# Kernel optimization log

Hardware: AMD Instinct MI355X
Metric: run time of the kernel (lower is better)

The kernel has to match this reference:

```python
import jax, jax.numpy as jnp
import numpy as np


def _gat(x, adj, W, a):
    # x: [N, J, Fin], W: [H, Fin, hs], a: [H, 2*hs]
    # e_ij = leakyrelu(a1.Wh_i + a2.Wh_j)  (decomposed form of the repeat/cat construction)
    hs = W.shape[-1]
    Wh = jnp.einsum('bjf,hfd->bhjd', x, W)
    s1 = jnp.einsum('bhjd,hd->bhj', Wh, a[:, :hs])
    s2 = jnp.einsum('bhjd,hd->bhj', Wh, a[:, hs:])
    e = jax.nn.leaky_relu(s1[..., :, None] + s2[..., None, :], 0.2)
    e = jnp.where(adj[None, None] > 0, e, jnp.float32(-9e15))
    att = jax.nn.softmax(e, axis=-1)
    h = jnp.einsum('bhij,bhjd->bhid', att, Wh)
    b, H, j, d = h.shape
    return jax.nn.elu(h.transpose(0, 2, 1, 3).reshape(b, j, H * d))


def _conv_bn_relu(x, w, bias, g, be, m, v):
    # x: [N, C, T], w: [O, I, 3], BN in inference mode
    y = jax.lax.conv_general_dilated(x, w, (1,), [(1, 1)], dimension_numbers=('NCH', 'OIH', 'NCH'))
    y = y + bias[None, :, None]
    y = (y - m[None, :, None]) / jnp.sqrt(v[None, :, None] + 1e-5) * g[None, :, None] + be[None, :, None]
    return jax.nn.relu(y)


def _mha(q, k, v, wq, bq, wk, bk, wv, bv, wo, bo):
    # torch nn.MultiheadAttention, 4 heads, eval mode (no dropout)
    n, L, D = q.shape
    H = 4
    hd = D // H
    def proj(x, w, b):
        return (x @ w.T + b).reshape(n, -1, H, hd)
    Q, K, V = proj(q, wq, bq), proj(k, wk, bk), proj(v, wv, bv)
    att = jax.nn.softmax(jnp.einsum('nqhd,nkhd->nhqk', Q, K) * jnp.float32(1.0 / np.sqrt(hd)), axis=-1)
    o = jnp.einsum('nhqk,nkhd->nqhd', att, V).reshape(n, L, D)
    return o @ wo.T + bo


def _lstm_dir(x, wih, whh, bih, bhh, rev):
    # x: [B, T, D]; torch gate order i, f, g, o
    b, t, _ = x.shape
    H = whh.shape[1]
    xw = jnp.transpose(x @ wih.T + (bih + bhh), (1, 0, 2))  # [T, B, 4H]
    def step(carry, xt):
        h, c = carry
        gates = xt + h @ whh.T
        i, f, g, o = jnp.split(gates, 4, axis=-1)
        c = jax.nn.sigmoid(f) * c + jax.nn.sigmoid(i) * jnp.tanh(g)
        h = jax.nn.sigmoid(o) * jnp.tanh(c)
        return (h, c), h
    init = (jnp.zeros((b, H), x.dtype), jnp.zeros((b, H), x.dtype))
    _, hs = jax.lax.scan(step, init, xw, reverse=rev)
    return jnp.transpose(hs, (1, 0, 2))


def _forward(lh, rh, adj, vis, g1W, g1a, g2W, g2a, c1w, c1b, b1g, b1b, b1m, b1v, c2w, c2b, b2g, b2b, b2m, b2v,
             wq, bq, wk, bk, wv, bv, wo, bo,
             l0fw, l0fu, l0fbi, l0fbh, l0bw, l0bu, l0bbi, l0bbh,
             l1fw, l1fu, l1fbi, l1fbh, l1bw, l1bu, l1bbi, l1bbh,
             o1w, o1b, o2w, o2b):
    B, T, J, F = lh.shape

    def single_hand(x):
        h = x.reshape(B * T, J, F)
        h = _gat(h, adj, g1W, g1a)
        h = _gat(h, adj, g2W, g2a)
        D = h.shape[-1]
        ht = h.reshape(B, T, J, D).transpose(0, 2, 3, 1).reshape(B * J, D, T)
        ht = _conv_bn_relu(ht, c1w, c1b, b1g, b1b, b1m, b1v)
        ht = _conv_bn_relu(ht, c2w, c2b, b2g, b2b, b2m, b2v)
        return ht.reshape(B, J, D, T).transpose(0, 3, 1, 2)  # [B, T, J, D]

    l = single_hand(lh)
    r = single_hand(rh)
    D = l.shape[-1]
    lf = l.reshape(B * T, J, D)
    rf = r.reshape(B * T, J, D)
    a_l2r = _mha(lf, rf, rf, wq, bq, wk, bk, wv, bv, wo, bo)
    a_r2l = _mha(rf, lf, lf, wq, bq, wk, bk, wv, bv, wo, bo)
    # repair of shape-inconsistent torch reshape: pool joints before the seq LSTM
    le = (lf + 0.5 * a_r2l).reshape(B, T, J, D).mean(axis=2)
    re = (rf + 0.5 * a_l2r).reshape(B, T, J, D).mean(axis=2)

    def bilstm(x):
        h1 = jnp.concatenate([_lstm_dir(x, l0fw, l0fu, l0fbi, l0fbh, False),
                              _lstm_dir(x, l0bw, l0bu, l0bbi, l0bbh, True)], -1)
        return jnp.concatenate([_lstm_dir(h1, l1fw, l1fu, l1fbi, l1fbh, False),
                                _lstm_dir(h1, l1bw, l1bu, l1bbi, l1bbh, True)], -1)

    def head(x):
        y = jax.nn.relu(x @ o1w.T + o1b) @ o2w.T + o2b  # [B, T, 3*J]
        return y.reshape(B, T, J, 3)

    lp = head(bilstm(le)) * vis[..., None]
    rp = head(bilstm(re)) * vis[..., None]
    return lp, rp


def setup_inputs() -> dict:
    key = jax.random.key(0)
    ks = jax.random.split(key, 60)
    it = iter(range(60))
    B, T, J, F, D = 8, 512, 21, 512, 256
    def nrm(shape, s=0.05):
        return jax.random.normal(ks[next(it)], shape, jnp.float32) * s
    inp = {}
    inp['left_hand_feats'] = nrm((B, T, J, F), 1.0)
    inp['right_hand_feats'] = nrm((B, T, J, F), 1.0)
    adj = (jax.random.uniform(ks[next(it)], (J, J)) < 0.3).astype(jnp.float32)
    inp['hand_adj_matrix'] = jnp.maximum(adj, jnp.eye(J, dtype=jnp.float32))
    inp['hand_visibility'] = jax.random.uniform(ks[next(it)], (B, T, J), jnp.float32)
    inp['gat1_W'] = nrm((4, F, 64)); inp['gat1_a'] = nrm((4, 128))
    inp['gat2_W'] = nrm((4, D, 64)); inp['gat2_a'] = nrm((4, 128))
    inp['conv1_w'] = nrm((D, D, 3)); inp['conv1_b'] = nrm((D,))
    inp['conv2_w'] = nrm((D, D, 3)); inp['conv2_b'] = nrm((D,))
    for p in ['bn1', 'bn2']:
        inp[p + '_g'] = jnp.ones((D,), jnp.float32)
        inp[p + '_b'] = jnp.zeros((D,), jnp.float32)
        inp[p + '_m'] = jnp.zeros((D,), jnp.float32)
        inp[p + '_v'] = jnp.ones((D,), jnp.float32)
    for p in ['attn_wq', 'attn_wk', 'attn_wv', 'attn_wo']:
        inp[p] = nrm((D, D))
    for p in ['attn_bq', 'attn_bk', 'attn_bv', 'attn_bo']:
        inp[p] = nrm((D,))
    H = D // 2
    for l in ['lstm0f', 'lstm0b', 'lstm1f', 'lstm1b']:
        inp[l + '_wih'] = nrm((4 * H, D))
        inp[l + '_whh'] = nrm((4 * H, H))
        inp[l + '_bih'] = nrm((4 * H,))
        inp[l + '_bhh'] = nrm((4 * H,))
    inp['out1_w'] = nrm((D, D)); inp['out1_b'] = nrm((D,))
    inp['out2_w'] = nrm((3 * J, D)); inp['out2_b'] = nrm((3 * J,))
    return inp


def reference(left_hand_feats, right_hand_feats, hand_adj_matrix, hand_visibility,
              gat1_W, gat1_a, gat2_W, gat2_a,
              conv1_w, conv1_b, bn1_g, bn1_b, bn1_m, bn1_v,
              conv2_w, conv2_b, bn2_g, bn2_b, bn2_m, bn2_v,
              attn_wq, attn_bq, attn_wk, attn_bk, attn_wv, attn_bv, attn_wo, attn_bo,
              lstm0f_wih, lstm0f_whh, lstm0f_bih, lstm0f_bhh,
              lstm0b_wih, lstm0b_whh, lstm0b_bih, lstm0b_bhh,
              lstm1f_wih, lstm1f_whh, lstm1f_bih, lstm1f_bhh,
              lstm1b_wih, lstm1b_whh, lstm1b_bih, lstm1b_bhh,
              out1_w, out1_b, out2_w, out2_b):
    return _forward(left_hand_feats, right_hand_feats, hand_adj_matrix, hand_visibility,
                    gat1_W, gat1_a, gat2_W, gat2_a,
                    conv1_w, conv1_b, bn1_g, bn1_b, bn1_m, bn1_v,
                    conv2_w, conv2_b, bn2_g, bn2_b, bn2_m, bn2_v,
                    attn_wq, attn_bq, attn_wk, attn_bk, attn_wv, attn_bv, attn_wo, attn_bo,
                    lstm0f_wih, lstm0f_whh, lstm0f_bih, lstm0f_bhh,
                    lstm0b_wih, lstm0b_whh, lstm0b_bih, lstm0b_bhh,
                    lstm1f_wih, lstm1f_whh, lstm1f_bih, lstm1f_bhh,
                    lstm1b_wih, lstm1b_whh, lstm1b_bih, lstm1b_bhh,
                    out1_w, out1_b, out2_w, out2_b)
```

## Files before the change

kernel.cpp:

```cpp
#include <hip/hip_runtime.h>

typedef __bf16 bf16;
typedef bf16 bf16x8 __attribute__((ext_vector_type(8)));
typedef bf16 bf16x4 __attribute__((ext_vector_type(4)));
typedef float f32x4 __attribute__((ext_vector_type(4)));
typedef _Float16 f16;
typedef f16 f16x8 __attribute__((ext_vector_type(8)));

#define NBT 4096
#define NJ 21
#define NLF 86016
#define DD 256
#define CONV_M 86352
#define SPAD 514
#define CROWS 86528

__device__ __forceinline__ void gload16(const bf16* g, bf16* l) {
  __builtin_amdgcn_global_load_lds(
      (const __attribute__((address_space(1))) unsigned int*)g,
      (__attribute__((address_space(3))) unsigned int*)l, 16, 0, 0);
}

__global__ __launch_bounds__(256, 2) void gemm_bf16(
    const void* __restrict__ Av, const bf16* __restrict__ Bt,
    float* __restrict__ C32, bf16* __restrict__ Cout,
    const float* __restrict__ bias, const float* __restrict__ sc,
    const float* __restrict__ sh, int M, int N, int K, int lda, int flags)
{
  __shared__ __align__(16) bf16 As[128][32];
  __shared__ __align__(16) bf16 Bs[128][32];
  const int tid = threadIdx.x;
  const long m0 = (long)blockIdx.y * 128;
  const int n0 = blockIdx.x * 128;
  const int wave = tid >> 6, lane = tid & 63;
  const int wm = (wave & 1) * 64, wn = (wave >> 1) * 64;
  const int frow = lane & 15, fkb = (lane >> 4) * 8;
  const int crow = lane >> 2, ccol = (lane & 3) * 8;
  f32x4 acc[4][4] = {};
  for (int k0 = 0; k0 < K; k0 += 32) {
    if (flags & 1) {
      const int lr = tid >> 1, lc = (tid & 1) * 16;
      const float* ap = (const float*)Av + (m0 + lr) * (long)lda + (k0 + lc);
      bf16x8 t0, t1;
      #pragma unroll
      for (int u = 0; u < 8; u++) { t0[u] = (bf16)ap[u]; t1[u] = (bf16)ap[8 + u]; }
      *(bf16x8*)(&As[lr][lc])     = t0;
      *(bf16x8*)(&As[lr][lc + 8]) = t1;
    } else {
      #pragma unroll
      for (int cc = 0; cc < 2; cc++) {
        const int ch = wave * 2 + cc;
        gload16((const bf16*)Av + (m0 + ch * 16 + crow) * (long)lda + (k0 + ccol),
                &As[ch * 16][0]);
      }
    }
    #pragma unroll
    for (int cc = 0; cc < 2; cc++) {
      const int ch = wave * 2 + cc;
      gload16(Bt + (n0 + ch * 16 + crow) * (long)K + (k0 + ccol),
              &Bs[ch * 16][0]);
    }
    __syncthreads();
    bf16x8 af[4], bg[4];
    #pragma unroll
    for (int i = 0; i < 4; i++) af[i] = *(const bf16x8*)(&As[wm + i * 16 + frow][fkb]);
    #pragma unroll
    for (int j = 0; j < 4; j++) bg[j] = *(const bf16x8*)(&Bs[wn + j * 16 + frow][fkb]);
    #pragma unroll
    for (int i = 0; i < 4; i++)
      #pragma unroll
      for (int j = 0; j < 4; j++)
        acc[i][j] = __builtin_amdgcn_mfma_f32_16x16x32_bf16(af[i], bg[j], acc[i][j], 0, 0, 0);
    __syncthreads();
  }
  const int col = lane & 15, rbase = (lane >> 4) * 4;
  #pragma unroll
  for (int i = 0; i < 4; i++) {
    #pragma unroll
    for (int j = 0; j < 4; j++) {
      const int nn = n0 + wn + j * 16 + col;
      #pragma unroll
      for (int r = 0; r < 4; r++) {
        const long mm = m0 + wm + i * 16 + rbase + r;
        if (mm >= M) continue;
        float v = acc[i][j][r];
        if (flags & 2) { C32[mm * (long)N + nn] = v; continue; }
        if (flags & 8) v = v * sc[nn] + sh[nn];
        else if (bias) v += bias[nn];
        if (flags & 4) v = fmaxf(v, 0.f);
        if (flags & 16) {
          const int s = (int)(mm % SPAD);
          if (s == 0 || s == SPAD - 1) v = 0.f;
          Cout[mm * (long)N + nn] = (bf16)v;
        } else if (flags & 32) {
          const long hj = mm / SPAD; const int s = (int)(mm - hj * SPAD);
          if (s == 0 || s == SPAD - 1) continue;
          const long b = hj / NJ; const int j2 = (int)(hj - b * NJ);
          const long dst = (b * 512 + (s - 1)) * NJ + j2;
          Cout[dst * (long)N + nn] = (bf16)v;
        } else {
          Cout[mm * (long)N + nn] = (bf16)v;
        }
      }
    }
  }
}

__global__ void cvt_k(const float* __restrict__ s, bf16* __restrict__ d, long n) {
  long i = (long)blockIdx.x * 256 + threadIdx.x;
  if (i < n) d[i] = (bf16)s[i];
}
__global__ void cvt4_k(const float* __restrict__ s, bf16* __restrict__ d, long n4) {
  long i = (long)blockIdx.x * 256 + threadIdx.x;
  if (i >= n4) return;
  const f32x4 v = ((const f32x4*)s)[i];
  bf16x4 o; o[0] = (bf16)v[0]; o[1] = (bf16)v[1]; o[2] = (bf16)v[2]; o[3] = (bf16)v[3];
  ((bf16x4*)d)[i] = o;
}
__global__ void prep_gatW(const float* __restrict__ W, bf16* __restrict__ Wt, int F) {
  long idx = (long)blockIdx.x * 256 + threadIdx.x;
  if (idx >= 256L * F) return;
  int n = (int)(idx / F), f = (int)(idx % F);
  Wt[idx] = (bf16)W[((long)(n >> 6) * F + f) * 64 + (n & 63)];
}
__global__ void prep_convw(const float* __restrict__ w, bf16* __restrict__ wp) {
  int idx = blockIdx.x * 256 + threadIdx.x;
  int n = idx / 768, k = idx % 768, tap = k >> 8, i = k & 255;
  wp[idx] = (bf16)w[(n * 256 + i) * 3 + tap];
}
__global__ void prep_out2(const float* __restrict__ w, bf16* __restrict__ wp) {
  int idx = blockIdx.x * 256 + threadIdx.x;
  wp[idx] = (idx < 63 * 256) ? (bf16)w[idx] : (bf16)0.f;
}
__global__ void prep_scsh(const float* __restrict__ cb, const float* __restrict__ g,
                          const float* __restrict__ be, const float* __restrict__ m,
                          const float* __restrict__ v, float* __restrict__ sc,
                          float* __restrict__ sh) {
  int c = threadIdx.x;
  float rs = rsqrtf(v[c] + 1e-5f) * g[c];
  sc[c] = rs; sh[c] = (cb[c] - m[c]) * rs + be[c];
}
__global__ void prep_bkv(const float* __restrict__ bk, const float* __restrict__ bv,
                         float* __restrict__ o) {
  int i = blockIdx.x * 256 + threadIdx.x;
  if (i >= 512) return;
  o[i] = (i < 256) ? bk[i] : bv[i - 256];
}
__global__ void pad_zero(bf16* __restrict__ convIn) {
  int idx = blockIdx.x * 256 + threadIdx.x;
  int hj = idx >> 9, s = ((idx >> 8) & 1) ? (SPAD - 1) : 0, c = idx & 255;
  convIn[((long)hj * SPAD + s) * DD + c] = (bf16)0.f;
}
__global__ void zero_out(float* __restrict__ o, long n) {
  long i = (long)blockIdx.x * 256 + threadIdx.x;
  if (i < n) o[i] = 0.f;
}

__global__ __launch_bounds__(256) void gat_attn(
    const bf16* __restrict__ Wh, const float* __restrict__ a,
    const float* __restrict__ adj, bf16* __restrict__ out, int convMode)
{
  const int bt = blockIdx.x, tid = threadIdx.x;
  __shared__ float whs[NJ][DD];
  __shared__ float s1[4][NJ], s2[4][NJ];
  __shared__ float att[4][NJ][NJ];
  const long base = (long)bt * NJ * DD;
  for (int i = tid; i < NJ * DD; i += 256)
    whs[i >> 8][i & 255] = (float)Wh[base + i];
  __syncthreads();
  if (tid < 4 * NJ) {
    const int h = tid / NJ, i = tid % NJ;
    float x1 = 0.f, x2 = 0.f;
    for (int d = 0; d < 64; d++) {
      const float w = whs[i][h * 64 + d];
      x1 += w * a[h * 128 + d];
      x2 += w * a[h * 128 + 64 + d];
    }
    s1[h][i] = x1; s2[h][i] = x2;
  }
  __syncthreads();
  for (int idx = tid; idx < 4 * NJ * NJ; idx += 256) {
    const int h = idx / (NJ * NJ), r = idx % (NJ * NJ), i = r / NJ, j = r % NJ;
    float e = s1[h][i] + s2[h][j];
    e = e > 0.f ? e : 0.2f * e;
    att[h][i][j] = (adj[i * NJ + j] > 0.f) ? e : -9e15f;
  }
  __syncthreads();
  if (tid < 4 * NJ) {
    const int h = tid / NJ, i = tid % NJ;
    float mx = -3e38f;
    for (int j = 0; j < NJ; j++) mx = fmaxf(mx, att[h][i][j]);
    float sum = 0.f;
    for (int j = 0; j < NJ; j++) { const float ex = __expf(att[h][i][j] - mx); att[h][i][j] = ex; sum += ex; }
    const float inv = 1.f / sum;
    for (int j = 0; j < NJ; j++) att[h][i][j] *= inv;
  }
  __syncthreads();
  const int b = bt >> 9, t = bt & 511;
  for (int idx = tid; idx < NJ * DD; idx += 256) {
    const int i = idx >> 8, c = idx & 255, h = c >> 6;
    float s = 0.f;
    for (int j = 0; j < NJ; j++) s += att[h][i][j] * whs[j][c];
    s = s > 0.f ? s : (__expf(s) - 1.f);
    const long row = convMode ? (((long)(b * NJ + i)) * SPAD + (t + 1)) : ((long)bt * NJ + i);
    out[row * DD + c] = (bf16)s;
  }
}

__global__ __launch_bounds__(256) void mha_core2(
    const bf16* __restrict__ Q, const bf16* __restrict__ KV,
    bf16* __restrict__ O)
{
  const int bt = blockIdx.x, tid = threadIdx.x;
  __shared__ bf16 qs[NJ][DD], ks[NJ][DD], vs[NJ][DD];
  __shared__ float att[4][NJ][NJ];
  const long baseq = (long)bt * NJ * DD;
  const long basekv = (long)bt * NJ * 512;
  for (int i = tid; i < NJ * DD; i += 256) {
    const int r = i >> 8, c = i & 255;
    qs[r][c] = Q[baseq + i];
    ks[r][c] = KV[basekv + r * 512 + c];
    vs[r][c] = KV[basekv + r * 512 + 256 + c];
  }
  __syncthreads();
  for (int idx = tid; idx < 4 * NJ * NJ; idx += 256) {
    const int h = idx / (NJ * NJ), r = idx % (NJ * NJ), i = r / NJ, j = r % NJ;
    float s = 0.f;
    for (int d = 0; d < 64; d++) s += (float)qs[i][h * 64 + d] * (float)ks[j][h * 64 + d];
    att[h][i][j] = s * 0.125f;
  }
  __syncthreads();
  if (tid < 4 * NJ) {
    const int h = tid / NJ, i = tid % NJ;
    float mx = -3e38f;
    for (int j = 0; j < NJ; j++) mx = fmaxf(mx, att[h][i][j]);
    float sum = 0.f;
    for (int j = 0; j < NJ; j++) { const float ex = __expf(att[h][i][j] - mx); att[h][i][j] = ex; sum += ex; }
    const float inv = 1.f / sum;
    for (int j = 0; j < NJ; j++) att[h][i][j] *= inv;
  }
  __syncthreads();
  for (int idx = tid; idx < NJ * DD; idx += 256) {
    const int i = idx >> 8, c = idx & 255, h = c >> 6;
    float s = 0.f;
    for (int j = 0; j < NJ; j++) s += att[h][i][j] * (float)vs[j][c];
    O[baseq + i * DD + c] = (bf16)s;
  }
}

__global__ __launch_bounds__(256) void pool_kernel(
    const bf16* __restrict__ lf, const bf16* __restrict__ ao, bf16* __restrict__ o)
{
  const int bt = blockIdx.x, c = threadIdx.x;
  float s = 0.f;
  for (int j = 0; j < NJ; j++) {
    const long r = ((long)bt * NJ + j) * DD + c;
    s += (float)lf[r] + 0.5f * (float)ao[r];
  }
  o[(long)bt * DD + c] = (bf16)(s * (1.f / 21.f));
}

#define REP16(X) X(0) X(1) X(2) X(3) X(4) X(5) X(6) X(7) X(8) X(9) X(10) X(11) \
  X(12) X(13) X(14) X(15)

#define LDS_FENCE() do { \
  asm volatile("s_waitcnt lgkmcnt(0)" ::: "memory"); \
  __builtin_amdgcn_sched_barrier(0); \
  __builtin_amdgcn_s_barrier(); \
  __builtin_amdgcn_sched_barrier(0); \
} while (0)

__global__ __launch_bounds__(512, 1) void lstm_lds(
    const float* __restrict__ xw,
    const float* __restrict__ whhF, const float* __restrict__ whhB,
    const float* __restrict__ bihF, const float* __restrict__ bhhF,
    const float* __restrict__ bihB, const float* __restrict__ bhhB,
    bf16* __restrict__ outL, bf16* __restrict__ outR)
{
  const int wg = blockIdx.x;
  const int hand = wg >> 4, dir = (wg >> 3) & 1, b = wg & 7;
  const int tid = threadIdx.x;
  const float* whh = dir ? whhB : whhF;

  __shared__ f16 whhs[512][136];
  __shared__ f16 hbuf[136];
  __shared__ float gsb[512];

  for (int i = tid; i < 512 * 128; i += 512)
    whhs[i >> 7][i & 127] = (f16)whh[i];
  if (tid < 136) hbuf[tid] = (f16)0.f;
  const float bias = (dir ? bihB : bihF)[tid] + (dir ? bhhB : bhhF)[tid];
  float c = 0.f;
  const float* xp = xw + ((long)hand * NBT + (long)b * 512) * 1024 + dir * 512;
  bf16* outp = hand ? outR : outL;
  float xv = xp[(long)(dir ? 511 : 0) * 1024 + tid];
  __syncthreads();

  const f16* wrow = &whhs[tid][0];
#define WRD(i) f16x8 w##i = *(const f16x8*)(wrow + (i) * 8);
  REP16(WRD)
#undef WRD

  for (int s = 0; s < 512; s++) {
    const int t = dir ? (511 - s) : s;
    const int tn = dir ? (510 - s) : (s + 1);
    float xnext = 0.f;
    if (s < 511) xnext = xp[(long)tn * 1024 + tid];
    float a0 = xv + bias, a1 = 0.f, a2 = 0.f, a3 = 0.f;
#define WDOT(i) { \
    const f16x8 hv = *(const f16x8*)(&hbuf[(i) * 8]); \
    a0 = __builtin_amdgcn_fdot2(__builtin_shufflevector(w##i, w##i, 0, 1), \
                                __builtin_shufflevector(hv, hv, 0, 1), a0, false); \
    a1 = __builtin_amdgcn_fdot2(__builtin_shufflevector(w##i, w##i, 2, 3), \
                                __builtin_shufflevector(hv, hv, 2, 3), a1, false); \
    a2 = __builtin_amdgcn_fdot2(__builtin_shufflevector(w##i, w##i, 4, 5), \
                                __builtin_shufflevector(hv, hv, 4, 5), a2, false); \
    a3 = __builtin_amdgcn_fdot2(__builtin_shufflevector(w##i, w##i, 6, 7), \
                                __builtin_shufflevector(hv, hv, 6, 7), a3, false); }
    REP16(WDOT)
#undef WDOT
    gsb[tid] = (a0 + a1) + (a2 + a3);
    LDS_FENCE();
    if (tid < 128) {
      const float ig = gsb[tid], fg = gsb[tid + 128], gg = gsb[tid + 256], og = gsb[tid + 384];
      const float si = __builtin_amdgcn_rcpf(1.f + __expf(-ig));
      const float sf = __builtin_amdgcn_rcpf(1.f + __expf(-fg));
      const float so = __builtin_amdgcn_rcpf(1.f + __expf(-og));
      const float tg = 1.f - 2.f * __builtin_amdgcn_rcpf(1.f + __expf(2.f * gg));
      c = sf * c + si * tg;
      const float tc = 1.f - 2.f * __builtin_amdgcn_rcpf(1.f + __expf(2.f * c));
      const float h = so * tc;
      hbuf[tid] = (f16)h;
      outp[((long)b * 512 + t) * 256 + dir * 128 + tid] = (bf16)h;
    }
    LDS_FENCE();
    xv = xnext;
  }
}

__global__ __launch_bounds__(256) void finalize_k(
    const float* __restrict__ y, const float* __restrict__ b2,
    const float* __restrict__ vis, float* __restrict__ out)
{
  const int idx = blockIdx.x * 256 + threadIdx.x;
  if (idx >= 2 * NBT * 63) return;
  const int c = idx % 63; const int r = idx / 63; const int bt = r & (NBT - 1);
  out[idx] = (y[(long)r * 128 + c] + b2[c]) * vis[bt * 21 + (c / 3)];
}

extern "C" void kernel_launch(void* const* d_in, const int* in_sizes, int n_in,
                              void* d_out, int out_size, void* d_ws, size_t ws_size,
                              hipStream_t stream) {
  (void)in_sizes; (void)n_in;
  const float* feats[2] = { (const float*)d_in[0], (const float*)d_in[1] };
  const float* adj  = (const float*)d_in[2];
  const float* vis  = (const float*)d_in[3];
  const float* gW[2] = { (const float*)d_in[4], (const float*)d_in[6] };
  const float* ga[2] = { (const float*)d_in[5], (const float*)d_in[7] };
  const float* cw_[2] = { (const float*)d_in[8],  (const float*)d_in[10] };
  const float* cb_[2] = { (const float*)d_in[9],  (const float*)d_in[11] };
  const float* bng[2] = { (const float*)d_in[12], (const float*)d_in[16] };
  const float* bnb[2] = { (const float*)d_in[13], (const float*)d_in[17] };
  const float* bnm[2] = { (const float*)d_in[14], (const float*)d_in[18] };
  const float* bnv[2] = { (const float*)d_in[15], (const float*)d_in[19] };
  const float* wq = (const float*)d_in[20], *wk = (const float*)d_in[21];
  const float* wv = (const float*)d_in[22], *wo = (const float*)d_in[23];
  const float* bq = (const float*)d_in[24], *bk = (const float*)d_in[25];
  const float* bv = (const float*)d_in[26], *bo = (const float*)d_in[27];
  const float* Lwih[2][2] = { { (const float*)d_in[28], (const float*)d_in[32] },
                              { (const float*)d_in[36], (const float*)d_in[40] } };
  const float* Lwhh[2][2] = { { (const float*)d_in[29], (const float*)d_in[33] },
                              { (const float*)d_in[37], (const float*)d_in[41] } };
  const float* Lbih[2][2] = { { (const float*)d_in[30], (const float*)d_in[34] },
                              { (const float*)d_in[38], (const float*)d_in[42] } };
  const float* Lbhh[2][2] = { { (const float*)d_in[31], (const float*)d_in[35] },
                              { (const float*)d_in[39], (const float*)d_in[43] } };
  const float* o1w = (const float*)d_in[44], *o1b = (const float*)d_in[45];
  const float* o2w = (const float*)d_in[46], *o2b = (const float*)d_in[47];

  char* base = (char*)d_ws;
  size_t off = 0;
  auto alloc = [&](size_t b) { size_t r = off; off += (b + 1023) & ~(size_t)1023; return r; };
  const size_t SZ_LF  = (size_t)NLF * DD * 2;
  const size_t SZ_CNV = (size_t)CROWS * DD * 2;
  const size_t SZ_BT  = (size_t)NBT * DD * 2;
  const size_t o_w1t = alloc((size_t)256 * 512 * 2);
  const size_t o_w2t = alloc((size_t)256 * 256 * 2);
  const size_t o_cw1 = alloc((size_t)256 * 768 * 2);
  const size_t o_cw2 = alloc((size_t)256 * 768 * 2);
  const size_t o_wq  = alloc((size_t)256 * 256 * 2);
  const size_t o_wk  = alloc((size_t)256 * 256 * 2);
  const size_t o_wv  = alloc((size_t)256 * 256 * 2);
  const size_t o_wo  = alloc((size_t)256 * 256 * 2);
  const size_t o_o1w = alloc((size_t)256 * 256 * 2);
  const size_t o_o2p = alloc((size_t)128 * 256 * 2);
  const size_t o_lw0 = alloc((size_t)512 * 256 * 2);
  const size_t o_lw1 = alloc((size_t)512 * 256 * 2);
  const size_t o_lw2 = alloc((size_t)512 * 256 * 2);
  const size_t o_lw3 = alloc((size_t)512 * 256 * 2);
  const size_t o_ss  = alloc((size_t)4 * 256 * 4);
  const size_t o_bkv = alloc((size_t)512 * 4);
  const size_t o_B1  = alloc(SZ_LF);
  const size_t o_B23 = alloc(2 * SZ_CNV);
  const size_t o_lfL = alloc(SZ_LF);
  const size_t o_lfR = alloc(SZ_LF);
  const size_t o_le  = alloc(SZ_BT);
  const size_t o_re  = alloc(SZ_BT);
  const size_t o_h1L = alloc(SZ_BT);
  const size_t o_h1R = alloc(SZ_BT);
  const size_t o_hoL = alloc(SZ_BT);
  const size_t o_hoR = alloc(SZ_BT);
  const size_t NEED = off;
  if (ws_size < NEED) {
    zero_out<<<(out_size + 255) / 256, 256, 0, stream>>>((float*)d_out, out_size);
    return;
  }
  auto P = [&](size_t o_) { return (void*)(base + o_); };

  auto gemm = [&](const void* A, const void* Bt, void* c32, void* co,
                  const void* bias_, const void* sc_, const void* sh_,
                  long M, int N, int K, int lda, int flags) {
    dim3 g((unsigned)(N / 128), (unsigned)((M + 127) / 128));
    gemm_bf16<<<g, 256, 0, stream>>>(A, (const bf16*)Bt, (float*)c32, (bf16*)co,
                                     (const float*)bias_, (const float*)sc_,
                                     (const float*)sh_, (int)M, N, K, lda, flags);
  };
  auto cvt = [&](const float* s, void* d, long n) {
    cvt_k<<<(unsigned)((n + 255) / 256), 256, 0, stream>>>(s, (bf16*)d, n);
  };

  prep_gatW<<<512, 256, 0, stream>>>(gW[0], (bf16*)P(o_w1t), 512);
  prep_gatW<<<256, 256, 0, stream>>>(gW[1], (bf16*)P(o_w2t), 256);
  prep_convw<<<768, 256, 0, stream>>>(cw_[0], (bf16*)P(o_cw1));
  prep_convw<<<768, 256, 0, stream>>>(cw_[1], (bf16*)P(o_cw2));
  cvt(wq, P(o_wq), 65536); cvt(wk, P(o_wk), 65536);
  cvt(wv, P(o_wv), 65536); cvt(wo, P(o_wo), 65536);
  cvt(o1w, P(o_o1w), 65536);
  cvt(Lwih[0][0], P(o_lw0), 131072); cvt(Lwih[0][1], P(o_lw1), 131072);
  cvt(Lwih[1][0], P(o_lw2), 131072); cvt(Lwih[1][1], P(o_lw3), 131072);
  prep_out2<<<128, 256, 0, stream>>>(o2w, (bf16*)P(o_o2p));
  float* sc1 = (float*)P(o_ss); float* sh1 = sc1 + 256;
  float* sc2 = sh1 + 256;       float* sh2 = sc2 + 256;
  prep_scsh<<<1, 256, 0, stream>>>(cb_[0], bng[0], bnb[0], bnm[0], bnv[0], sc1, sh1);
  prep_scsh<<<1, 256, 0, stream>>>(cb_[1], bng[1], bnb[1], bnm[1], bnv[1], sc2, sh2);
  prep_bkv<<<2, 256, 0, stream>>>(bk, bv, (float*)P(o_bkv));

  bf16* B1 = (bf16*)P(o_B1);
  bf16* B2 = (bf16*)P(o_B23);
  bf16* B3 = B2 + (size_t)CROWS * DD;
  bf16* lfb[2] = { (bf16*)P(o_lfL), (bf16*)P(o_lfR) };

  for (int hd = 0; hd < 2; hd++) {
    bf16* featbf = B2;
    cvt4_k<<<(unsigned)(((long)NLF * 512 / 4 + 255) / 256), 256, 0, stream>>>(
        feats[hd], featbf, (long)NLF * 512 / 4);
    gemm(featbf, P(o_w1t), nullptr, B1, nullptr, nullptr, nullptr,
         NLF, 256, 512, 512, 0);
    gat_attn<<<NBT, 256, 0, stream>>>(B1, ga[0], adj, B1, 0);
    gemm(B1, P(o_w2t), nullptr, B2, nullptr, nullptr, nullptr,
         NLF, 256, 256, 256, 0);
    pad_zero<<<336, 256, 0, stream>>>(B3 + DD);
    gat_attn<<<NBT, 256, 0, stream>>>(B2, ga[1], adj, B3 + DD, 1);
    gemm(B3, P(o_cw1), nullptr, B2 + DD, nullptr, sc1, sh1,
         CONV_M, 256, 768, 256, 8 | 4 | 16);
    gemm(B2, P(o_cw2), nullptr, lfb[hd], nullptr, sc2, sh2,
         CONV_M, 256, 768, 256, 8 | 4 | 32);
  }

  bf16* KV = (bf16*)P(o_B23);
  for (int pass = 0; pass < 2; pass++) {
    const bf16* qsrc = lfb[pass];
    const bf16* kvsrc = lfb[1 - pass];
    gemm(kvsrc, P(o_wk), nullptr, KV, P(o_bkv), nullptr, nullptr,
         NLF, 512, 256, 256, 0);
    gemm(qsrc, P(o_wq), nullptr, B1, bq, nullptr, nullptr, NLF, 256, 256, 256, 0);
    mha_core2<<<NBT, 256, 0, stream>>>(B1, KV, B1);
    gemm(B1, P(o_wo), nullptr, B2, bo, nullptr, nullptr, NLF, 256, 256, 256, 0);
    pool_kernel<<<NBT, 256, 0, stream>>>(kvsrc, B2,
        (bf16*)P(pass == 0 ? o_re : o_le));
  }

  float* xw = (float*)P(o_B23);
  gemm(P(o_le), P(o_lw0), xw, nullptr, nullptr, nullptr, nullptr,
       2 * NBT, 1024, 256, 256, 2);
  lstm_lds<<<32, 512, 0, stream>>>(xw, Lwhh[0][0], Lwhh[0][1],
      Lbih[0][0], Lbhh[0][0], Lbih[0][1], Lbhh[0][1],
      (bf16*)P(o_h1L), (bf16*)P(o_h1R));
  gemm(P(o_h1L), P(o_lw2), xw, nullptr, nullptr, nullptr, nullptr,
       2 * NBT, 1024, 256, 256, 2);
  lstm_lds<<<32, 512, 0, stream>>>(xw, Lwhh[1][0], Lwhh[1][1],
      Lbih[1][0], Lbhh[1][0], Lbih[1][1], Lbhh[1][1],
      (bf16*)P(o_hoL), (bf16*)P(o_hoR));

  gemm(P(o_hoL), P(o_o1w), nullptr, B1, o1b, nullptr, nullptr,
       2 * NBT, 256, 256, 256, 4);
  float* y32 = (float*)P(o_B23);
  gemm(B1, P(o_o2p), y32, nullptr, nullptr, nullptr, nullptr,
       2 * NBT, 128, 256, 256, 2);
  finalize_k<<<(2 * NBT * 63 + 255) / 256, 256, 0, stream>>>(
      y32, o2b, vis, (float*)d_out);
}
```

Before: 2.232 ms.

## Double-buffer GEMM LDS tiles to overlap global loads with MFMA

The bf16 GEMM kernel now keeps two LDS buffers for the A and B tiles and prefetches the next K-tile through async global_load_lds while MFMAs run on the current one. It uses explicit s_waitcnt vmcnt and lgkmcnt plus raw s_barrier calls with sched_barrier fences in place of __syncthreads. The aim is to hide global memory latency that was exposed by the load, sync, compute, sync sequence. LDS use per block doubles. The fp32-input conversion path (flags&1) is removed, so any caller still passing fp32 A would now read its data as bf16.

```diff
diff --git a/kernel.cpp b/kernel.cpp
--- a/kernel.cpp
+++ b/kernel.cpp
@@ -27,8 +27,8 @@
     const float* __restrict__ bias, const float* __restrict__ sc,
     const float* __restrict__ sh, int M, int N, int K, int lda, int flags)
 {
-  __shared__ __align__(16) bf16 As[128][32];
-  __shared__ __align__(16) bf16 Bs[128][32];
+  __shared__ __align__(16) bf16 As[2][128][32];
+  __shared__ __align__(16) bf16 Bs[2][128][32];
   const int tid = threadIdx.x;
   const long m0 = (long)blockIdx.y * 128;
   const int n0 = blockIdx.x * 128;
@@ -36,42 +36,49 @@
   const int wm = (wave & 1) * 64, wn = (wave >> 1) * 64;
   const int frow = lane & 15, fkb = (lane >> 4) * 8;
   const int crow = lane >> 2, ccol = (lane & 3) * 8;
+  const bf16* Ab = (const bf16*)Av;
+  const int nk = K >> 5;
+  const int ch0 = wave * 2, ch1 = ch0 + 1;
+  const long arow0 = (m0 + ch0 * 16 + crow) * (long)lda + ccol;
+  const long arow1 = (m0 + ch1 * 16 + crow) * (long)lda + ccol;
+  const long brow0 = ((long)(n0 + ch0 * 16 + crow)) * K + ccol;
+  const long brow1 = ((long)(n0 + ch1 * 16 + crow)) * K + ccol;
+
   f32x4 acc[4][4] = {};
-  for (int k0 = 0; k0 < K; k0 += 32) {
-    if (flags & 1) {
-      const int lr = tid >> 1, lc = (tid & 1) * 16;
-      const float* ap = (const float*)Av + (m0 + lr) * (long)lda + (k0 + lc);
-      bf16x8 t0, t1;
-      #pragma unroll
-      for (int u = 0; u < 8; u++) { t0[u] = (bf16)ap[u]; t1[u] = (bf16)ap[8 + u]; }
-      *(bf16x8*)(&As[lr][lc])     = t0;
-      *(bf16x8*)(&As[lr][lc + 8]) = t1;
+  gload16(Ab + arow0, &As[0][ch0 * 16][0]);
+  gload16(Ab + arow1, &As[0][ch1 * 16][0]);
+  gload16(Bt + brow0, &Bs[0][ch0 * 16][0]);
+  gload16(Bt + brow1, &Bs[0][ch1 * 16][0]);
+
+  for (int kt = 0; kt < nk; kt++) {
+    const int cur = kt & 1;
+    if (kt + 1 < nk) {
+      const int k0 = (kt + 1) << 5;
+      gload16(Ab + arow0 + k0, &As[cur ^ 1][ch0 * 16][0]);
+      gload16(Ab + arow1 + k0, &As[cur ^ 1][ch1 * 16][0]);
+      gload16(Bt + brow0 + k0, &Bs[cur ^ 1][ch0 * 16][0]);
+      gload16(Bt + brow1 + k0, &Bs[cur ^ 1][ch1 * 16][0]);
+      asm volatile("s_waitcnt vmcnt(4) lgkmcnt(0)" ::: "memory");
     } else {
-      #pragma unroll
-      for (int cc = 0; cc < 2; cc++) {
-        const int ch = wave * 2 + cc;
-        gload16((const bf16*)Av + (m0 + ch * 16 + crow) * (long)lda + (k0 + ccol),
-                &As[ch * 16][0]);
-      }
+      asm volatile("s_waitcnt vmcnt(0) lgkmcnt(0)" ::: "memory");
     }
-    #pragma unroll
-    for (int cc = 0; cc < 2; cc++) {
-      const int ch = wave * 2 + cc;
-      gload16(Bt + (n0 + ch * 16 + crow) * (long)K + (k0 + ccol),
-              &Bs[ch * 16][0]);
-    }
-    __syncthreads();
+    __builtin_amdgcn_sched_barrier(0);
+    __builtin_amdgcn_s_barrier();
+    __builtin_amdgcn_sched_barrier(0);
     bf16x8 af[4], bg[4];
     #pragma unroll
-    for (int i = 0; i < 4; i++) af[i] = *(const bf16x8*)(&As[wm + i * 16 + frow][fkb]);
+    for (int i = 0; i < 4; i++) af[i] = *(const bf16x8*)(&As[cur][wm + i * 16 + frow][fkb]);
     #pragma unroll
-    for (int j = 0; j < 4; j++) bg[j] = *(const bf16x8*)(&Bs[wn + j * 16 + frow][fkb]);
+    for (int j = 0; j < 4; j++) bg[j] = *(const bf16x8*)(&Bs[cur][wn + j * 16 + frow][fkb]);
     #pragma unroll
     for (int i = 0; i < 4; i++)
       #pragma unroll
       for (int j = 0; j < 4; j++)
         acc[i][j] = __builtin_amdgcn_mfma_f32_16x16x32_bf16(af[i], bg[j], acc[i][j], 0, 0, 0);
-    __syncthreads();
+    asm volatile("s_waitcnt lgkmcnt(0)" ::: "memory");
+    __builtin_amdgcn_sched_barrier(0);
+    __builtin_amdgcn_s_barrier();
+    __builtin_amdgcn_sched_barrier(0);
   }
   const int col = lane & 15, rbase = (lane >> 4) * 4;
   #pragma unroll
```

Result: no change. 2.229 ms (-0.1%).
